# Optimization experiments

Measured on AMD Instinct MI355X. Metric: run time of the kernel, lower is better.

The kernel has to match this reference:

```python
import jax, jax.numpy as jnp
import numpy as np

NEG_SLOPE = 0.2  # PyG GATConv default negative_slope
BN_EPS = 1e-5


def _segment_softmax(logits, seg, num_segments):
    # numerically stable softmax over edges grouped by destination node
    m = jax.ops.segment_max(logits, seg, num_segments=num_segments)
    e = jnp.exp(logits - m[seg])
    s = jax.ops.segment_sum(e, seg, num_segments=num_segments)
    return e / s[seg]


def _gat_conv(x, src, dst, W, a_src, a_dst, bias, heads, d_head, concat):
    N = x.shape[0]
    h = (x @ W).reshape(N, heads, d_head)                      # [N, H, D]
    alpha_src = jnp.einsum('nhd,hd->nh', h, a_src)             # [N, H]
    alpha_dst = jnp.einsum('nhd,hd->nh', h, a_dst)             # [N, H]
    logits = jax.nn.leaky_relu(alpha_src[src] + alpha_dst[dst], NEG_SLOPE)  # [E, H]
    alpha = _segment_softmax(logits, dst, N)                   # [E, H]
    msg = h[src] * alpha[:, :, None]                           # [E, H, D]
    out = jax.ops.segment_sum(msg, dst, num_segments=N)        # [N, H, D]
    out = out.reshape(N, heads * d_head) if concat else out.mean(axis=1)
    return out + bias


def setup_inputs() -> dict:
    key = jax.random.key(0)
    ks = jax.random.split(key, 12)
    N, E = 50000, 800000
    in_dim, hidden, out_dim, heads = 256, 128, 2, 4
    d1 = hidden // heads  # 32
    s = 0.05
    return {
        'x': jax.random.normal(ks[0], (N, in_dim), dtype=jnp.float32),
        'edge_index': jax.random.randint(ks[1], (2, E), 0, N, dtype=jnp.int64),
        'W1': jax.random.normal(ks[2], (in_dim, heads * d1), dtype=jnp.float32) * s,
        'att_src1': jax.random.normal(ks[3], (heads, d1), dtype=jnp.float32) * s,
        'att_dst1': jax.random.normal(ks[4], (heads, d1), dtype=jnp.float32) * s,
        'b1': jnp.zeros((heads * d1,), dtype=jnp.float32),
        'bn_gamma': jnp.ones((hidden,), dtype=jnp.float32),
        'bn_beta': jnp.zeros((hidden,), dtype=jnp.float32),
        'bn_mean': jnp.zeros((hidden,), dtype=jnp.float32),
        'bn_var': jnp.ones((hidden,), dtype=jnp.float32),
        'W2': jax.random.normal(ks[5], (hidden, out_dim), dtype=jnp.float32) * s,
        'att_src2': jax.random.normal(ks[6], (1, out_dim), dtype=jnp.float32) * s,
        'att_dst2': jax.random.normal(ks[7], (1, out_dim), dtype=jnp.float32) * s,
        'b2': jnp.zeros((out_dim,), dtype=jnp.float32),
    }


def reference(x, edge_index, W1, att_src1, att_dst1, b1,
              bn_gamma, bn_beta, bn_mean, bn_var,
              W2, att_src2, att_dst2, b2):
    N = x.shape[0]
    # PyG GATConv adds self-loops by default
    loop = jnp.arange(N, dtype=edge_index.dtype)
    src = jnp.concatenate([edge_index[0], loop])
    dst = jnp.concatenate([edge_index[1], loop])

    heads, d1 = att_src1.shape
    h = _gat_conv(x, src, dst, W1, att_src1, att_dst1, b1, heads, d1, concat=True)
    # BatchNorm1d in eval mode (running stats), then ReLU (dropout is a no-op in eval)
    h = (h - bn_mean) * jax.lax.rsqrt(bn_var + BN_EPS) * bn_gamma + bn_beta
    h = jax.nn.relu(h)
    out = _gat_conv(h, src, dst, W2, att_src2, att_dst2, b2, 1, att_src2.shape[1], concat=False)
    return out
```

## Files before the change

kernel.cpp:

```cpp
#include <hip/hip_runtime.h>
#include <hip/hip_bf16.h>

#define LRELU(x) ((x) > 0.f ? (x) : 0.2f * (x))
#define CAP 96
#define BINBITS 7
#define BINCAP 2600

typedef short bf16x8 __attribute__((ext_vector_type(8)));
typedef float f32x4 __attribute__((ext_vector_type(4)));

__device__ __forceinline__ float b2f(unsigned short u) {
  union { unsigned int i; float f; } v;
  v.i = ((unsigned int)u) << 16;
  return v.f;
}
__device__ __forceinline__ unsigned short f2b(float f) {
  unsigned int u = __float_as_uint(f);
  unsigned int r = (u + 0x7fffu + ((u >> 16) & 1u)) >> 16;
  return (unsigned short)r;
}

__global__ __launch_bounds__(256) void prep_w1t_kernel(
    const float* __restrict__ W, unsigned short* __restrict__ w1t) {
  int idx = blockIdx.x * 256 + threadIdx.x;
  int n = idx >> 8, k = idx & 255;
  w1t[idx] = f2b(W[k * 128 + n]);
}

__global__ __launch_bounds__(256) void gemm1_mfma_kernel(
    const float* __restrict__ x, const unsigned short* __restrict__ w1t,
    const float* __restrict__ atts, const float* __restrict__ attd,
    unsigned short* __restrict__ h1bf, float* __restrict__ asrc,
    float* __restrict__ adst, int N) {
  __shared__ unsigned short bsh[128 * 264];

  const int tid = threadIdx.x;
#pragma unroll
  for (int i = 0; i < 16; i++) {
    int idx = (i * 256 + tid) * 8;
    int row = idx >> 8;
    int k = idx & 255;
    *(uint4*)(bsh + row * 264 + k) = *(const uint4*)(w1t + row * 256 + k);
  }
  __syncthreads();

  const int m0 = blockIdx.x * 64 + (tid >> 6) * 16;
  if (m0 >= N) return;
  const int lane = tid & 63;
  const int row = lane & 15;
  const int quad = lane >> 4;

  f32x4 acc[8];
#pragma unroll
  for (int t = 0; t < 8; t++) acc[t] = (f32x4){0.f, 0.f, 0.f, 0.f};

  const float* ap = x + (size_t)(m0 + row) * 256 + quad * 8;
#pragma unroll
  for (int k0 = 0; k0 < 256; k0 += 32) {
    float4 av0 = *(const float4*)(ap + k0);
    float4 av1 = *(const float4*)(ap + k0 + 4);
    float af[8] = {av0.x, av0.y, av0.z, av0.w, av1.x, av1.y, av1.z, av1.w};
    bf16x8 ahi, alo;
#pragma unroll
    for (int j = 0; j < 8; j++) {
      unsigned short h = f2b(af[j]);
      ahi[j] = (short)h;
      alo[j] = (short)f2b(af[j] - b2f(h));
    }
#pragma unroll
    for (int t = 0; t < 8; t++) {
      bf16x8 b = *(const bf16x8*)(bsh + (t * 16 + row) * 264 + k0 + quad * 8);
      acc[t] = __builtin_amdgcn_mfma_f32_16x16x32_bf16(ahi, b, acc[t], 0, 0, 0);
      acc[t] = __builtin_amdgcn_mfma_f32_16x16x32_bf16(alo, b, acc[t], 0, 0, 0);
    }
  }
  unsigned short* op = h1bf + (size_t)(m0 + quad * 4) * 128 + row;
#pragma unroll
  for (int t = 0; t < 8; t++)
#pragma unroll
    for (int r = 0; r < 4; r++)
      op[(size_t)r * 128 + t * 16] = f2b(acc[t][r]);

  float asv[8], adv[8];
#pragma unroll
  for (int t = 0; t < 8; t++) {
    asv[t] = atts[t * 16 + row];
    adv[t] = attd[t * 16 + row];
  }
  float ps[4][4], pd[4][4];
#pragma unroll
  for (int h = 0; h < 4; h++)
#pragma unroll
    for (int r = 0; r < 4; r++) {
      ps[h][r] = acc[2 * h][r] * asv[2 * h] + acc[2 * h + 1][r] * asv[2 * h + 1];
      pd[h][r] = acc[2 * h][r] * adv[2 * h] + acc[2 * h + 1][r] * adv[2 * h + 1];
    }
#pragma unroll
  for (int o = 1; o < 16; o <<= 1) {
#pragma unroll
    for (int h = 0; h < 4; h++)
#pragma unroll
      for (int r = 0; r < 4; r++) {
        ps[h][r] += __shfl_xor(ps[h][r], o);
        pd[h][r] += __shfl_xor(pd[h][r], o);
      }
  }
  if (row == 0) {
#pragma unroll
    for (int r = 0; r < 4; r++) {
      int m = m0 + quad * 4 + r;
#pragma unroll
      for (int h = 0; h < 4; h++) {
        asrc[m * 4 + h] = ps[h][r];
        adst[m * 4 + h] = pd[h][r];
      }
    }
  }
}

__global__ __launch_bounds__(256) void bin_edges_kernel(
    const int* __restrict__ ei, int E, int* __restrict__ gcnt,
    unsigned int* __restrict__ binned, int nbins) {
  __shared__ int hist[512];
  __shared__ int base[512];
  const int tid = threadIdx.x;
  for (int i = tid; i < 512; i += 256) hist[i] = 0;
  __syncthreads();
  const int chunk = (E + gridDim.x - 1) / gridDim.x;
  const int e0 = blockIdx.x * chunk;
  const int e1 = min(e0 + chunk, E);
  for (int e = e0 + tid; e < e1; e += 256)
    atomicAdd(&hist[ei[(size_t)E + e] >> BINBITS], 1);
  __syncthreads();
  for (int i = tid; i < nbins; i += 256)
    if (hist[i] > 0) base[i] = atomicAdd(&gcnt[i], hist[i]);
  __syncthreads();
  for (int i = tid; i < 512; i += 256) hist[i] = 0;
  __syncthreads();
  for (int e = e0 + tid; e < e1; e += 256) {
    int s = ei[e];
    int t = ei[(size_t)E + e];
    int b = t >> BINBITS;
    int pos = base[b] + atomicAdd(&hist[b], 1);
    if (pos < BINCAP)
      binned[(size_t)b * BINCAP + pos] = ((unsigned int)t << 16) | (unsigned int)s;
  }
}

__global__ __launch_bounds__(256) void bin_to_buckets_kernel(
    const int* __restrict__ gcnt, const unsigned int* __restrict__ binned,
    int* __restrict__ cnt, unsigned short* __restrict__ buckets, int N) {
  __shared__ unsigned short lbkt[128 * CAP];
  __shared__ int lcnt[128];
  const int b = blockIdx.x;
  const int tid = threadIdx.x;
  if (tid < 128) lcnt[tid] = 0;
  __syncthreads();
  const int ne = min(gcnt[b], BINCAP);
  const unsigned int* bp = binned + (size_t)b * BINCAP;
  for (int i = tid; i < ne; i += 256) {
    unsigned int p = bp[i];
    int ln = (p >> 16) & 127;
    int pos = atomicAdd(&lcnt[ln], 1);
    if (pos < CAP) lbkt[ln * CAP + pos] = (unsigned short)(p & 0xffff);
  }
  __syncthreads();
  const int n0 = b << BINBITS;
  const int nn = min(128, N - n0);
  if (nn <= 0) return;
  if (tid < nn) cnt[n0 + tid] = lcnt[tid];
  const int total8 = (nn * CAP) >> 3;
  uint4* d4 = (uint4*)(buckets + (size_t)n0 * CAP);
  const uint4* s4 = (const uint4*)lbkt;
  for (int i = tid; i < total8; i += 256) d4[i] = s4[i];
}

__global__ __launch_bounds__(256) void agg1_kernel(
    const int* __restrict__ cnt, const unsigned short* __restrict__ buckets,
    const unsigned short* __restrict__ h1bf, const float* __restrict__ asrc,
    const float* __restrict__ adst, const float* __restrict__ b1,
    const float* __restrict__ gamma, const float* __restrict__ beta,
    const float* __restrict__ mean, const float* __restrict__ var,
    const float* __restrict__ W2, const float* __restrict__ as2,
    const float* __restrict__ ad2, float4* __restrict__ pk, int N) {
  const int t = blockIdx.x * 4 + (threadIdx.x >> 6);
  if (t >= N) return;
  const int l = threadIdx.x & 63;
  const int h = l >> 4;
  const float ad = adst[t * 4 + h];

  float acc0 = 0.f, acc1 = 0.f, den = 0.f;
  const unsigned short* bkt = buckets + (size_t)t * CAP;
  const int deg = min(cnt[t], CAP);
  int j = 0;
  for (; j + 4 <= deg; j += 4) {
    int s0 = bkt[j], s1 = bkt[j + 1];
    int s2 = bkt[j + 2], s3 = bkt[j + 3];
    unsigned int p0 = *(const unsigned int*)(h1bf + (size_t)s0 * 128 + 2 * l);
    unsigned int p1 = *(const unsigned int*)(h1bf + (size_t)s1 * 128 + 2 * l);
    unsigned int p2 = *(const unsigned int*)(h1bf + (size_t)s2 * 128 + 2 * l);
    unsigned int p3 = *(const unsigned int*)(h1bf + (size_t)s3 * 128 + 2 * l);
    float w0 = __expf(LRELU(asrc[s0 * 4 + h] + ad));
    float w1 = __expf(LRELU(asrc[s1 * 4 + h] + ad));
    float w2 = __expf(LRELU(asrc[s2 * 4 + h] + ad));
    float w3 = __expf(LRELU(asrc[s3 * 4 + h] + ad));
    acc0 += w0 * b2f((unsigned short)(p0 & 0xffff)) +
            w1 * b2f((unsigned short)(p1 & 0xffff)) +
            w2 * b2f((unsigned short)(p2 & 0xffff)) +
            w3 * b2f((unsigned short)(p3 & 0xffff));
    acc1 += w0 * b2f((unsigned short)(p0 >> 16)) +
            w1 * b2f((unsigned short)(p1 >> 16)) +
            w2 * b2f((unsigned short)(p2 >> 16)) +
            w3 * b2f((unsigned short)(p3 >> 16));
    den += w0 + w1 + w2 + w3;
  }
  for (; j < deg; j++) {
    int s0 = bkt[j];
    unsigned int p0 = *(const unsigned int*)(h1bf + (size_t)s0 * 128 + 2 * l);
    float w0 = __expf(LRELU(asrc[s0 * 4 + h] + ad));
    acc0 += w0 * b2f((unsigned short)(p0 & 0xffff));
    acc1 += w0 * b2f((unsigned short)(p0 >> 16));
    den += w0;
  }
  {
    unsigned int p0 = *(const unsigned int*)(h1bf + (size_t)t * 128 + 2 * l);
    float w0 = __expf(LRELU(asrc[t * 4 + h] + ad));
    acc0 += w0 * b2f((unsigned short)(p0 & 0xffff));
    acc1 += w0 * b2f((unsigned short)(p0 >> 16));
    den += w0;
  }
  const int c0 = 2 * l;
  float inv = 1.f / den;
  float v0 = acc0 * inv + b1[c0];
  float v1 = acc1 * inv + b1[c0 + 1];
  v0 = (v0 - mean[c0]) * rsqrtf(var[c0] + 1e-5f) * gamma[c0] + beta[c0];
  v1 = (v1 - mean[c0 + 1]) * rsqrtf(var[c0 + 1] + 1e-5f) * gamma[c0 + 1] +
       beta[c0 + 1];
  v0 = v0 > 0.f ? v0 : 0.f;
  v1 = v1 > 0.f ? v1 : 0.f;

  float g0 = v0 * W2[c0 * 2 + 0] + v1 * W2[(c0 + 1) * 2 + 0];
  float g1 = v0 * W2[c0 * 2 + 1] + v1 * W2[(c0 + 1) * 2 + 1];
#pragma unroll
  for (int o = 32; o > 0; o >>= 1) {
    g0 += __shfl_down(g0, o);
    g1 += __shfl_down(g1, o);
  }
  if (l == 0) {
    float4 p;
    p.x = g0;
    p.y = g1;
    p.z = g0 * as2[0] + g1 * as2[1];
    p.w = g0 * ad2[0] + g1 * ad2[1];
    pk[t] = p;
  }
}

__global__ __launch_bounds__(256) void agg2_kernel(
    const int* __restrict__ cnt, const unsigned short* __restrict__ buckets,
    const float4* __restrict__ pk, const float* __restrict__ b2,
    float* __restrict__ out, int N) {
  const int t = blockIdx.x * 16 + (threadIdx.x >> 4);
  if (t >= N) return;
  const int lg = threadIdx.x & 15;
  float4 pt = pk[t];
  const float ad = pt.w;
  float a0 = 0.f, a1 = 0.f, den = 0.f;
  const unsigned short* bkt = buckets + (size_t)t * CAP;
  const int deg = min(cnt[t], CAP);
  for (int j = lg; j < deg; j += 16) {
    float4 p = pk[bkt[j]];
    float w = __expf(LRELU(p.z + ad));
    a0 += w * p.x;
    a1 += w * p.y;
    den += w;
  }
#pragma unroll
  for (int o = 8; o > 0; o >>= 1) {
    a0 += __shfl_xor(a0, o);
    a1 += __shfl_xor(a1, o);
    den += __shfl_xor(den, o);
  }
  if (lg == 0) {
    float w = __expf(LRELU(pt.z + ad));
    a0 += w * pt.x;
    a1 += w * pt.y;
    den += w;
    float2 o2;
    o2.x = a0 / den + b2[0];
    o2.y = a1 / den + b2[1];
    *(float2*)(out + (size_t)t * 2) = o2;
  }
}

extern "C" void kernel_launch(void* const* d_in, const int* in_sizes, int n_in,
                              void* d_out, int out_size, void* d_ws,
                              size_t ws_size, hipStream_t stream) {
  const float* x      = (const float*)d_in[0];
  const int*   ei     = (const int*)d_in[1];
  const float* W1     = (const float*)d_in[2];
  const float* atts1  = (const float*)d_in[3];
  const float* attd1  = (const float*)d_in[4];
  const float* b1     = (const float*)d_in[5];
  const float* gamma  = (const float*)d_in[6];
  const float* beta   = (const float*)d_in[7];
  const float* mean   = (const float*)d_in[8];
  const float* var    = (const float*)d_in[9];
  const float* W2     = (const float*)d_in[10];
  const float* atts2  = (const float*)d_in[11];
  const float* attd2  = (const float*)d_in[12];
  const float* b2     = (const float*)d_in[13];
  float* out = (float*)d_out;

  const int N = in_sizes[0] / 256;
  const int E = in_sizes[1] / 2;
  const int nbins = (N + (1 << BINBITS) - 1) >> BINBITS;

  char* ws = (char*)d_ws;
  size_t off = 0;
  unsigned short* h1bf = (unsigned short*)(ws + off); off += (size_t)N * 128 * 2;
  float* asrc1 = (float*)(ws + off); off += (size_t)N * 4 * 4;
  float* adst1 = (float*)(ws + off); off += (size_t)N * 4 * 4;
  float4* pk   = (float4*)(ws + off); off += (size_t)N * 16;
  int*   cnt   = (int*)  (ws + off); off += (size_t)N * 4;
  int*   gcnt  = (int*)  (ws + off); off += 512 * 4;
  unsigned short* w1t = (unsigned short*)(ws + off); off += 128 * 256 * 2;
  unsigned short* buckets = (unsigned short*)(ws + off);
  off += (size_t)N * CAP * 2;
  unsigned int* binned = (unsigned int*)(ws + off);
  off += (size_t)nbins * BINCAP * 4;

  hipMemsetAsync(gcnt, 0, 512 * 4, stream);
  bin_edges_kernel<<<512, 256, 0, stream>>>(ei, E, gcnt, binned, nbins);
  bin_to_buckets_kernel<<<nbins, 256, 0, stream>>>(gcnt, binned, cnt, buckets,
                                                   N);

  prep_w1t_kernel<<<128, 256, 0, stream>>>(W1, w1t);
  gemm1_mfma_kernel<<<(N + 63) / 64, 256, 0, stream>>>(
      x, w1t, atts1, attd1, h1bf, asrc1, adst1, N);
  agg1_kernel<<<(N + 3) / 4, 256, 0, stream>>>(cnt, buckets, h1bf, asrc1,
                                               adst1, b1, gamma, beta, mean,
                                               var, W2, atts2, attd2, pk, N);

  agg2_kernel<<<(N + 15) / 16, 256, 0, stream>>>(cnt, buckets, pk, b2, out, N);
}
```

Before: 209.1 us.

## Stage binned edges in LDS, amortize W1 tile over rows, scalarize agg1 indices

bin_edges now sorts each fixed-size chunk of edges by bin in shared memory, using a prefix scan and a staging buffer, before writing them to global memory. This makes the global writes contiguous per bin instead of scattered. The GEMM1 kernel now processes 256 rows per block in four sub-tiles, so the W1 copy into LDS is amortized over more rows, with clamping for tail rows. agg1 uses readfirstlane on degree and neighbour indices so they stay in scalar registers, and it adds a larger LDS footprint in bin_edges that may lower occupancy.

Measured after the change: 227.6 us. +8.8%, slower.

```diff
diff --git a/kernel.cpp b/kernel.cpp
--- a/kernel.cpp
+++ b/kernel.cpp
@@ -5,6 +5,8 @@
 #define CAP 96
 #define BINBITS 7
 #define BINCAP 2600
+#define NBINS_MAX 512
+#define CHUNKA 6272
 
 typedef short bf16x8 __attribute__((ext_vector_type(8)));
 typedef float f32x4 __attribute__((ext_vector_type(4)));
@@ -44,42 +46,10 @@
   }
   __syncthreads();
 
-  const int m0 = blockIdx.x * 64 + (tid >> 6) * 16;
-  if (m0 >= N) return;
   const int lane = tid & 63;
   const int row = lane & 15;
   const int quad = lane >> 4;
-
-  f32x4 acc[8];
-#pragma unroll
-  for (int t = 0; t < 8; t++) acc[t] = (f32x4){0.f, 0.f, 0.f, 0.f};
-
-  const float* ap = x + (size_t)(m0 + row) * 256 + quad * 8;
-#pragma unroll
-  for (int k0 = 0; k0 < 256; k0 += 32) {
-    float4 av0 = *(const float4*)(ap + k0);
-    float4 av1 = *(const float4*)(ap + k0 + 4);
-    float af[8] = {av0.x, av0.y, av0.z, av0.w, av1.x, av1.y, av1.z, av1.w};
-    bf16x8 ahi, alo;
-#pragma unroll
-    for (int j = 0; j < 8; j++) {
-      unsigned short h = f2b(af[j]);
-      ahi[j] = (short)h;
-      alo[j] = (short)f2b(af[j] - b2f(h));
-    }
-#pragma unroll
-    for (int t = 0; t < 8; t++) {
-      bf16x8 b = *(const bf16x8*)(bsh + (t * 16 + row) * 264 + k0 + quad * 8);
-      acc[t] = __builtin_amdgcn_mfma_f32_16x16x32_bf16(ahi, b, acc[t], 0, 0, 0);
-      acc[t] = __builtin_amdgcn_mfma_f32_16x16x32_bf16(alo, b, acc[t], 0, 0, 0);
-    }
-  }
-  unsigned short* op = h1bf + (size_t)(m0 + quad * 4) * 128 + row;
-#pragma unroll
-  for (int t = 0; t < 8; t++)
-#pragma unroll
-    for (int r = 0; r < 4; r++)
-      op[(size_t)r * 128 + t * 16] = f2b(acc[t][r]);
+  const int wv = tid >> 6;
 
   float asv[8], adv[8];
 #pragma unroll
@@ -87,32 +57,76 @@
     asv[t] = atts[t * 16 + row];
     adv[t] = attd[t * 16 + row];
   }
-  float ps[4][4], pd[4][4];
-#pragma unroll
-  for (int h = 0; h < 4; h++)
-#pragma unroll
-    for (int r = 0; r < 4; r++) {
-      ps[h][r] = acc[2 * h][r] * asv[2 * h] + acc[2 * h + 1][r] * asv[2 * h + 1];
-      pd[h][r] = acc[2 * h][r] * adv[2 * h] + acc[2 * h + 1][r] * adv[2 * h + 1];
+
+  for (int rt = 0; rt < 4; rt++) {
+    const int m0 = blockIdx.x * 256 + rt * 64 + wv * 16;
+    if (m0 >= N) break;
+
+    f32x4 acc[8];
+#pragma unroll
+    for (int t = 0; t < 8; t++) acc[t] = (f32x4){0.f, 0.f, 0.f, 0.f};
+
+    const int rclamp = min(m0 + row, N - 1);
+    const float* ap = x + (size_t)rclamp * 256 + quad * 8;
+#pragma unroll
+    for (int k0 = 0; k0 < 256; k0 += 32) {
+      float4 av0 = *(const float4*)(ap + k0);
+      float4 av1 = *(const float4*)(ap + k0 + 4);
+      float af[8] = {av0.x, av0.y, av0.z, av0.w, av1.x, av1.y, av1.z, av1.w};
+      bf16x8 ahi, alo;
+#pragma unroll
+      for (int j = 0; j < 8; j++) {
+        unsigned short h = f2b(af[j]);
+        ahi[j] = (short)h;
+        alo[j] = (short)f2b(af[j] - b2f(h));
+      }
+#pragma unroll
+      for (int t = 0; t < 8; t++) {
+        bf16x8 b = *(const bf16x8*)(bsh + (t * 16 + row) * 264 + k0 + quad * 8);
+        acc[t] =
+            __builtin_amdgcn_mfma_f32_16x16x32_bf16(ahi, b, acc[t], 0, 0, 0);
+        acc[t] =
+            __builtin_amdgcn_mfma_f32_16x16x32_bf16(alo, b, acc[t], 0, 0, 0);
+      }
     }
-#pragma unroll
-  for (int o = 1; o < 16; o <<= 1) {
+    unsigned short* op = h1bf + (size_t)(m0 + quad * 4) * 128 + row;
+#pragma unroll
+    for (int t = 0; t < 8; t++)
+#pragma unroll
+      for (int r = 0; r < 4; r++)
+        if (m0 + quad * 4 + r < N) op[(size_t)r * 128 + t * 16] = f2b(acc[t][r]);
+
+    float ps[4][4], pd[4][4];
 #pragma unroll
     for (int h = 0; h < 4; h++)
 #pragma unroll
       for (int r = 0; r < 4; r++) {
-        ps[h][r] += __shfl_xor(ps[h][r], o);
-        pd[h][r] += __shfl_xor(pd[h][r], o);
+        ps[h][r] =
+            acc[2 * h][r] * asv[2 * h] + acc[2 * h + 1][r] * asv[2 * h + 1];
+        pd[h][r] =
+            acc[2 * h][r] * adv[2 * h] + acc[2 * h + 1][r] * adv[2 * h + 1];
       }
-  }
-  if (row == 0) {
-#pragma unroll
-    for (int r = 0; r < 4; r++) {
-      int m = m0 + quad * 4 + r;
-#pragma unroll
-      for (int h = 0; h < 4; h++) {
-        asrc[m * 4 + h] = ps[h][r];
-        adst[m * 4 + h] = pd[h][r];
+#pragma unroll
+    for (int o = 1; o < 16; o <<= 1) {
+#pragma unroll
+      for (int h = 0; h < 4; h++)
+#pragma unroll
+        for (int r = 0; r < 4; r++) {
+          ps[h][r] += __shfl_xor(ps[h][r], o);
+          pd[h][r] += __shfl_xor(pd[h][r], o);
+        }
+    }
+    if (row == 0) {
+#pragma unroll
+      for (int r = 0; r < 4; r++) {
+        int m = m0 + quad * 4 + r;
+        if (m < N) {
+#pragma unroll
+          for (int h = 0; h < 4; h++) {
+            asrc[m * 4 + h] = ps[h][r];
+            adst[m * 4 + h] = pd[h][r];
+          }
+        }
       }
     }
   }
@@ -121,29 +135,51 @@
 __global__ __launch_bounds__(256) void bin_edges_kernel(
     const int* __restrict__ ei, int E, int* __restrict__ gcnt,
     unsigned int* __restrict__ binned, int nbins) {
-  __shared__ int hist[512];
-  __shared__ int base[512];
+  __shared__ int hist[NBINS_MAX];
+  __shared__ int lofs[NBINS_MAX];
+  __shared__ int gbase[NBINS_MAX];
+  __shared__ int cur[NBINS_MAX];
+  __shared__ unsigned int stage[CHUNKA];
   const int tid = threadIdx.x;
-  for (int i = tid; i < 512; i += 256) hist[i] = 0;
-  __syncthreads();
-  const int chunk = (E + gridDim.x - 1) / gridDim.x;
-  const int e0 = blockIdx.x * chunk;
-  const int e1 = min(e0 + chunk, E);
+  const int e0 = blockIdx.x * CHUNKA;
+  const int e1 = min(e0 + CHUNKA, E);
+
+  for (int i = tid; i < NBINS_MAX; i += 256) hist[i] = 0;
+  __syncthreads();
   for (int e = e0 + tid; e < e1; e += 256)
     atomicAdd(&hist[ei[(size_t)E + e] >> BINBITS], 1);
   __syncthreads();
-  for (int i = tid; i < nbins; i += 256)
-    if (hist[i] > 0) base[i] = atomicAdd(&gcnt[i], hist[i]);
-  __syncthreads();
-  for (int i = tid; i < 512; i += 256) hist[i] = 0;
+  for (int i = tid; i < NBINS_MAX; i += 256) {
+    gbase[i] = hist[i] ? atomicAdd(&gcnt[i], hist[i]) : 0;
+    lofs[i] = hist[i];
+  }
+  __syncthreads();
+  for (int off = 1; off < NBINS_MAX; off <<= 1) {
+    int i0 = tid, i1 = tid + 256;
+    int v0 = (i0 >= off) ? lofs[i0 - off] : 0;
+    int v1 = (i1 >= off) ? lofs[i1 - off] : 0;
+    __syncthreads();
+    lofs[i0] += v0;
+    lofs[i1] += v1;
+    __syncthreads();
+  }
+  for (int i = tid; i < NBINS_MAX; i += 256) cur[i] = lofs[i] - hist[i];
   __syncthreads();
   for (int e = e0 + tid; e < e1; e += 256) {
     int s = ei[e];
     int t = ei[(size_t)E + e];
     int b = t >> BINBITS;
-    int pos = base[b] + atomicAdd(&hist[b], 1);
-    if (pos < BINCAP)
-      binned[(size_t)b * BINCAP + pos] = ((unsigned int)t << 16) | (unsigned int)s;
+    int idx = atomicAdd(&cur[b], 1);
+    stage[idx] = ((unsigned int)t << 16) | (unsigned int)s;
+  }
+  __syncthreads();
+  const int ne = e1 - e0;
+  for (int i = tid; i < ne; i += 256) {
+    unsigned int p = stage[i];
+    int b = p >> (16 + BINBITS);
+    int excl = lofs[b] - hist[b];
+    int gpos = gbase[b] + (i - excl);
+    if (gpos < BINCAP) binned[(size_t)b * BINCAP + gpos] = p;
   }
 }
 
@@ -183,7 +219,8 @@
     const float* __restrict__ mean, const float* __restrict__ var,
     const float* __restrict__ W2, const float* __restrict__ as2,
     const float* __restrict__ ad2, float4* __restrict__ pk, int N) {
-  const int t = blockIdx.x * 4 + (threadIdx.x >> 6);
+  const int wv = __builtin_amdgcn_readfirstlane(threadIdx.x >> 6);
+  const int t = blockIdx.x * 4 + wv;
   if (t >= N) return;
   const int l = threadIdx.x & 63;
   const int h = l >> 4;
@@ -191,11 +228,13 @@
 
   float acc0 = 0.f, acc1 = 0.f, den = 0.f;
   const unsigned short* bkt = buckets + (size_t)t * CAP;
-  const int deg = min(cnt[t], CAP);
+  const int deg = min(__builtin_amdgcn_readfirstlane(cnt[t]), CAP);
   int j = 0;
   for (; j + 4 <= deg; j += 4) {
-    int s0 = bkt[j], s1 = bkt[j + 1];
-    int s2 = bkt[j + 2], s3 = bkt[j + 3];
+    int s0 = __builtin_amdgcn_readfirstlane((int)bkt[j]);
+    int s1 = __builtin_amdgcn_readfirstlane((int)bkt[j + 1]);
+    int s2 = __builtin_amdgcn_readfirstlane((int)bkt[j + 2]);
+    int s3 = __builtin_amdgcn_readfirstlane((int)bkt[j + 3]);
     unsigned int p0 = *(const unsigned int*)(h1bf + (size_t)s0 * 128 + 2 * l);
     unsigned int p1 = *(const unsigned int*)(h1bf + (size_t)s1 * 128 + 2 * l);
     unsigned int p2 = *(const unsigned int*)(h1bf + (size_t)s2 * 128 + 2 * l);
@@ -215,7 +254,7 @@
     den += w0 + w1 + w2 + w3;
   }
   for (; j < deg; j++) {
-    int s0 = bkt[j];
+    int s0 = __builtin_amdgcn_readfirstlane((int)bkt[j]);
     unsigned int p0 = *(const unsigned int*)(h1bf + (size_t)s0 * 128 + 2 * l);
     float w0 = __expf(LRELU(asrc[s0 * 4 + h] + ad));
     acc0 += w0 * b2f((unsigned short)(p0 & 0xffff));
@@ -323,20 +362,21 @@
   float* adst1 = (float*)(ws + off); off += (size_t)N * 4 * 4;
   float4* pk   = (float4*)(ws + off); off += (size_t)N * 16;
   int*   cnt   = (int*)  (ws + off); off += (size_t)N * 4;
-  int*   gcnt  = (int*)  (ws + off); off += 512 * 4;
+  int*   gcnt  = (int*)  (ws + off); off += NBINS_MAX * 4;
   unsigned short* w1t = (unsigned short*)(ws + off); off += 128 * 256 * 2;
   unsigned short* buckets = (unsigned short*)(ws + off);
   off += (size_t)N * CAP * 2;
   unsigned int* binned = (unsigned int*)(ws + off);
   off += (size_t)nbins * BINCAP * 4;
 
-  hipMemsetAsync(gcnt, 0, 512 * 4, stream);
-  bin_edges_kernel<<<512, 256, 0, stream>>>(ei, E, gcnt, binned, nbins);
+  hipMemsetAsync(gcnt, 0, NBINS_MAX * 4, stream);
+  bin_edges_kernel<<<(E + CHUNKA - 1) / CHUNKA, 256, 0, stream>>>(
+      ei, E, gcnt, binned, nbins);
   bin_to_buckets_kernel<<<nbins, 256, 0, stream>>>(gcnt, binned, cnt, buckets,
                                                    N);
 
   prep_w1t_kernel<<<128, 256, 0, stream>>>(W1, w1t);
-  gemm1_mfma_kernel<<<(N + 63) / 64, 256, 0, stream>>>(
+  gemm1_mfma_kernel<<<(N + 255) / 256, 256, 0, stream>>>(
       x, w1t, atts1, attd1, h1bf, asrc1, adst1, N);
   agg1_kernel<<<(N + 3) / 4, 256, 0, stream>>>(cnt, buckets, h1bf, asrc1,
                                                adst1, b1, gamma, beta, mean,
```
